# Kernel tuning notes

Hardware: AMD Instinct MI355X
Metric: run time of the kernel (lower is better)

The kernel has to match this reference:

```python
import jax, jax.numpy as jnp
import numpy as np

B, T, E, V, U = 4096, 80, 100, 10000, 1024


def setup_inputs() -> dict:
    key = jax.random.key(0)
    ks = jax.random.split(key, 8)
    def w(k, shape, fan_in):
        return jax.random.normal(k, shape, jnp.float32) * (1.0 / np.sqrt(fan_in))
    return {
        "inputs": jax.random.randint(ks[0], (B, T), 0, V, dtype=jnp.int32),
        "emb_table": w(ks[1], (V, E), E),
        "Wx0": w(ks[2], (E, U), E),
        "Wh0": w(ks[3], (U, U), U),
        "b0": jnp.zeros((U,), jnp.float32),
        "Wx1": w(ks[4], (U, U), U),
        "Wh1": w(ks[5], (U, U), U),
        "b1": jnp.zeros((U,), jnp.float32),
        "Wfc": w(ks[6], (U, 1), U),
        "bfc": jnp.zeros((1,), jnp.float32),
    }


def reference(inputs, emb_table, Wx0, Wh0, b0, Wx1, Wh1, b1, Wfc, bfc):
    # Embedding lookup: [B, T, E]
    x = emb_table[inputs]
    # Time-major for scan: [T, B, E]
    xs = jnp.swapaxes(x, 0, 1)
    h0_init = jnp.zeros((inputs.shape[0], Wh0.shape[0]), x.dtype)
    h1_init = jnp.zeros((inputs.shape[0], Wh1.shape[0]), x.dtype)

    def step(carry, xt):
        h0, h1 = carry
        # SimpleRNNCell: h' = tanh(x @ Wx + h @ Wh + b); output == new state
        h0 = jnp.tanh(xt @ Wx0 + h0 @ Wh0 + b0)
        h1 = jnp.tanh(h0 @ Wx1 + h1 @ Wh1 + b1)
        return (h0, h1), None

    (h0, h1), _ = jax.lax.scan(step, (h0_init, h1_init), xs)
    # Final dense + sigmoid on last layer-1 output
    prob = jax.nn.sigmoid(h1 @ Wfc + bfc)
    return prob
```

## Files before the change

kernel.cpp:

```cpp
#include <hip/hip_runtime.h>
#include <stdint.h>

#define B_ 4096
#define T_ 80
#define E_ 100
#define V_ 10000
#define U_ 1024

typedef unsigned short u16;
typedef __attribute__((ext_vector_type(8))) __bf16 bf16x8;
typedef __attribute__((ext_vector_type(4))) float f32x4;

__device__ __forceinline__ float bf2f(u16 u) {
    union { unsigned int i; float f; } v; v.i = ((unsigned int)u) << 16; return v.f;
}
__device__ __forceinline__ u16 f2bf(float f) {
    union { float f; unsigned int i; } v; v.f = f;
    unsigned int x = v.i;
    return (u16)((x + 0x7fffu + ((x >> 16) & 1u)) >> 16);
}

__device__ __forceinline__ void load16(const void* g, void* l) {
    __builtin_amdgcn_global_load_lds(
        (__attribute__((address_space(1))) void*)(uintptr_t)g,
        (__attribute__((address_space(3))) void*)(uint32_t)(uintptr_t)l,
        16, 0, 0);
}

__global__ void transpose_pad(const float* __restrict__ src, u16* __restrict__ dst,
                              int K, int N, int Kp)
{
    __shared__ u16 tile[32][33];
    const int k0 = blockIdx.x * 32;
    const int n0 = blockIdx.y * 32;
    const int tx = threadIdx.x & 31;
    const int ty = threadIdx.x >> 5;
#pragma unroll
    for (int i = 0; i < 4; i++) {
        int k = k0 + ty + i * 8;
        tile[ty + i * 8][tx] = (k < K) ? f2bf(src[(size_t)k * N + (n0 + tx)]) : (u16)0;
    }
    __syncthreads();
#pragma unroll
    for (int i = 0; i < 4; i++) {
        int n = n0 + ty + i * 8;
        dst[(size_t)n * Kp + (k0 + tx)] = tile[tx][ty + i * 8];
    }
}

__global__ void embed_pad(const float* __restrict__ emb, u16* __restrict__ dst)
{
    int id = blockIdx.x * 256 + threadIdx.x;
    int v = id >> 7, k = id & 127;
    dst[id] = (k < E_) ? f2bf(emb[v * E_ + k]) : (u16)0;
}

__global__ void __launch_bounds__(256, 2)
rnn_phase(const u16* __restrict__ embP, const int* __restrict__ idx,
          const u16* __restrict__ Wx0T, const u16* __restrict__ Wh0T, const float* __restrict__ b0,
          const u16* __restrict__ Wx1T, const u16* __restrict__ Wh1T, const float* __restrict__ b1,
          const u16* __restrict__ h0r, u16* __restrict__ h0w,
          const u16* __restrict__ h1r, u16* __restrict__ h1w,
          int do0, int do1)
{
    const int linear = blockIdx.x;
    const int layer  = linear >> 8;
    if (layer ? !do1 : !do0) return;

    __shared__ u16 As[2][128 * 64];
    __shared__ u16 Bs[2][128 * 64];
    const int tid  = threadIdx.x;
    const int lane = tid & 63;
    const int wave = tid >> 6;
    const int wm = wave >> 1, wn = wave & 1;
    const int sub = linear & 255;
    const int m0 = (sub & 31) * 128;
    const int n0 = (sub >> 5) * 128;

    const u16 *A1, *W1, *A2, *W2; const float* bias; u16* C; int K1; bool gather;
    if (layer == 0) { A1 = embP; W1 = Wx0T; K1 = 128;  gather = true;  A2 = h0r; W2 = Wh0T; bias = b0; C = h0w; }
    else            { A1 = h0r;  W1 = Wx1T; K1 = 1024; gather = false; A2 = h1r; W2 = Wh1T; bias = b1; C = h1w; }
    const int KB1 = K1 >> 6;
    const int TOT = KB1 + (U_ >> 6);

    const int r8 = lane >> 3;
    const int c8 = lane & 7;

    int gv[4];
    if (gather) {
#pragma unroll
        for (int cc = 0; cc < 4; cc++)
            gv[cc] = idx[(size_t)(m0 + wave * 32 + cc * 8 + r8) * T_];
    }

    const f32x4 z = {0.f, 0.f, 0.f, 0.f};
    f32x4 acc[4][4];
#pragma unroll
    for (int i = 0; i < 4; i++)
#pragma unroll
        for (int j = 0; j < 4; j++) acc[i][j] = z;

    const int l15 = lane & 15, q = lane >> 4, l7 = lane & 7;
    int offA[2][4], offB[2][4];
#pragma unroll
    for (int kk = 0; kk < 2; kk++) {
#pragma unroll
        for (int f = 0; f < 4; f++) {
            const int rA = wm * 64 + f * 16 + l15;
            const int rB = wn * 64 + f * 16 + l15;
            offA[kk][f] = rA * 64 + (((kk * 4 + q) ^ l7) * 8);
            offB[kk][f] = rB * 64 + (((kk * 4 + q) ^ l7) * 8);
        }
    }

    auto stage = [&](int u, int p) {
        u16* Ad = As[p] + wave * 2048;
        u16* Bd = Bs[p] + wave * 2048;
        if (u < KB1) {
            const int k0 = u * 64;
#pragma unroll
            for (int cc = 0; cc < 4; cc++) {
                const int row = wave * 32 + cc * 8 + r8;
                const int scw = (c8 ^ (row & 7)) * 8;
                const u16* ap = gather ? A1 + (size_t)gv[cc] * 128 + k0 + scw
                                       : A1 + (size_t)(m0 + row) * K1 + k0 + scw;
                load16(ap, Ad + cc * 512);
                load16(W1 + (size_t)(n0 + row) * K1 + k0 + scw, Bd + cc * 512);
            }
        } else {
            const int k0 = (u - KB1) * 64;
#pragma unroll
            for (int cc = 0; cc < 4; cc++) {
                const int row = wave * 32 + cc * 8 + r8;
                const int scw = (c8 ^ (row & 7)) * 8;
                load16(A2 + (size_t)(m0 + row) * U_ + k0 + scw, Ad + cc * 512);
                load16(W2 + (size_t)(n0 + row) * U_ + k0 + scw, Bd + cc * 512);
            }
        }
    };

    stage(0, 0);

#pragma unroll 1
    for (int u = 0; u < TOT; ++u) {
        const int p = u & 1;
        __syncthreads();
        if (u + 1 < TOT) stage(u + 1, p ^ 1);
#pragma unroll
        for (int kk = 0; kk < 2; kk++) {
            bf16x8 a[4], b[4];
#pragma unroll
            for (int f = 0; f < 4; f++) {
                a[f] = *reinterpret_cast<const bf16x8*>(As[p] + offA[kk][f]);
                b[f] = *reinterpret_cast<const bf16x8*>(Bs[p] + offB[kk][f]);
            }
#pragma unroll
            for (int i = 0; i < 4; i++)
#pragma unroll
                for (int j = 0; j < 4; j++)
                    acc[i][j] = __builtin_amdgcn_mfma_f32_16x16x32_bf16(a[i], b[j], acc[i][j], 0, 0, 0);
        }
    }

#pragma unroll
    for (int j = 0; j < 4; j++) {
        const int col = n0 + wn * 64 + j * 16 + l15;
        const float bv = bias[col];
#pragma unroll
        for (int i = 0; i < 4; i++) {
#pragma unroll
            for (int r = 0; r < 4; r++) {
                const int row = m0 + wm * 64 + i * 16 + (q << 2) + r;
                float x = acc[i][j][r] + bv;
                x = fminf(15.f, fmaxf(-15.f, x));
                float e = __expf(2.f * x);
                C[(size_t)row * U_ + col] = f2bf((e - 1.f) / (e + 1.f));
            }
        }
    }
}

__global__ void final_dense(const u16* __restrict__ h1, const float* __restrict__ Wfc,
                            const float* __restrict__ bfc, float* __restrict__ out)
{
    const int lane = threadIdx.x & 63;
    const int wave = threadIdx.x >> 6;
    const int row = blockIdx.x * 4 + wave;
    const u16* hp = h1 + (size_t)row * U_ + lane * 16;
    const float* wp = Wfc + lane * 16;
    float s = 0.f;
#pragma unroll
    for (int i = 0; i < 16; i++) s += bf2f(hp[i]) * wp[i];
#pragma unroll
    for (int off = 32; off; off >>= 1) s += __shfl_down(s, off);
    if (lane == 0) {
        float x = s + bfc[0];
        out[row] = 1.f / (1.f + __expf(-x));
    }
}

extern "C" void kernel_launch(void* const* d_in, const int* in_sizes, int n_in,
                              void* d_out, int out_size, void* d_ws, size_t ws_size,
                              hipStream_t stream)
{
    const int*   inputs = (const int*)d_in[0];
    const float* emb    = (const float*)d_in[1];
    const float* Wx0    = (const float*)d_in[2];
    const float* Wh0    = (const float*)d_in[3];
    const float* b0     = (const float*)d_in[4];
    const float* Wx1    = (const float*)d_in[5];
    const float* Wh1    = (const float*)d_in[6];
    const float* b1     = (const float*)d_in[7];
    const float* Wfc    = (const float*)d_in[8];
    const float* bfc    = (const float*)d_in[9];

    char* ws = (char*)d_ws;
    const size_t MB = 1 << 20;
    u16* h0b[2] = { (u16*)(ws + 0 * MB), (u16*)(ws + 8 * MB) };
    u16* h1b[2] = { (u16*)(ws + 16 * MB), (u16*)(ws + 24 * MB) };
    u16* embP = (u16*)(ws + 32 * MB);
    u16* Wx0T = (u16*)(ws + 35 * MB);
    u16* Wh0T = (u16*)(ws + 36 * MB);
    u16* Wx1T = (u16*)(ws + 38 * MB);
    u16* Wh1T = (u16*)(ws + 40 * MB);

    hipMemsetAsync(h0b[1], 0, 8 * MB, stream);
    hipMemsetAsync(h1b[1], 0, 8 * MB, stream);

    embed_pad<<<V_ * 128 / 256, 256, 0, stream>>>(emb, embP);
    transpose_pad<<<dim3(128 / 32, U_ / 32), 256, 0, stream>>>(Wx0, Wx0T, E_, U_, 128);
    transpose_pad<<<dim3(U_ / 32, U_ / 32), 256, 0, stream>>>(Wh0, Wh0T, U_, U_, U_);
    transpose_pad<<<dim3(U_ / 32, U_ / 32), 256, 0, stream>>>(Wx1, Wx1T, U_, U_, U_);
    transpose_pad<<<dim3(U_ / 32, U_ / 32), 256, 0, stream>>>(Wh1, Wh1T, U_, U_, U_);

    for (int p = 0; p <= T_; ++p) {
        const int e = p & 1;
        rnn_phase<<<512, 256, 0, stream>>>(embP, inputs + p,
                                           Wx0T, Wh0T, b0, Wx1T, Wh1T, b1,
                                           h0b[e ^ 1], h0b[e], h1b[e], h1b[e ^ 1],
                                           (int)(p < T_), (int)(p >= 1));
    }
    final_dense<<<B_ / 4, 256, 0, stream>>>(h1b[1], Wfc, bfc, (float*)d_out);
}
```

Before: 2.762 ms.

## Deepen GEMM pipeline to four LDS stages with K-tile 32 and explicit waitcnt

The K tile shrinks from 64 to 32 and the LDS ring grows from 2 to 4 buffers, keeping three tiles in flight ahead of compute. Each iteration waits only on the oldest outstanding async global-to-LDS loads via explicit vmcnt before a raw barrier, so memory latency overlaps with MFMA work. The XOR swizzle is redone for 32-wide rows. The cost is twice as many barriers per tile and fragile hand-counted vmcnt values that depend on the compiler's exact load count.

Result: slower. 3.320 ms (+20.2%).

```diff
diff --git a/kernel.cpp b/kernel.cpp
--- a/kernel.cpp
+++ b/kernel.cpp
@@ -67,8 +67,8 @@
     const int layer  = linear >> 8;
     if (layer ? !do1 : !do0) return;
 
-    __shared__ u16 As[2][128 * 64];
-    __shared__ u16 Bs[2][128 * 64];
+    __shared__ u16 As[4][128 * 32];
+    __shared__ u16 Bs[4][128 * 32];
     const int tid  = threadIdx.x;
     const int lane = tid & 63;
     const int wave = tid >> 6;
@@ -80,17 +80,17 @@
     const u16 *A1, *W1, *A2, *W2; const float* bias; u16* C; int K1; bool gather;
     if (layer == 0) { A1 = embP; W1 = Wx0T; K1 = 128;  gather = true;  A2 = h0r; W2 = Wh0T; bias = b0; C = h0w; }
     else            { A1 = h0r;  W1 = Wx1T; K1 = 1024; gather = false; A2 = h1r; W2 = Wh1T; bias = b1; C = h1w; }
-    const int KB1 = K1 >> 6;
-    const int TOT = KB1 + (U_ >> 6);
-
-    const int r8 = lane >> 3;
-    const int c8 = lane & 7;
-
-    int gv[4];
+    const int KB1 = K1 >> 5;
+    const int TOT = KB1 + (U_ >> 5);
+
+    const int r4 = lane >> 2;
+    const int c4 = lane & 3;
+
+    int gv[2];
     if (gather) {
 #pragma unroll
-        for (int cc = 0; cc < 4; cc++)
-            gv[cc] = idx[(size_t)(m0 + wave * 32 + cc * 8 + r8) * T_];
+        for (int cc = 0; cc < 2; cc++)
+            gv[cc] = idx[(size_t)(m0 + wave * 32 + cc * 16 + r4) * T_];
     }
 
     const f32x4 z = {0.f, 0.f, 0.f, 0.f};
@@ -100,66 +100,66 @@
 #pragma unroll
         for (int j = 0; j < 4; j++) acc[i][j] = z;
 
-    const int l15 = lane & 15, q = lane >> 4, l7 = lane & 7;
-    int offA[2][4], offB[2][4];
-#pragma unroll
-    for (int kk = 0; kk < 2; kk++) {
-#pragma unroll
-        for (int f = 0; f < 4; f++) {
-            const int rA = wm * 64 + f * 16 + l15;
-            const int rB = wn * 64 + f * 16 + l15;
-            offA[kk][f] = rA * 64 + (((kk * 4 + q) ^ l7) * 8);
-            offB[kk][f] = rB * 64 + (((kk * 4 + q) ^ l7) * 8);
-        }
-    }
-
-    auto stage = [&](int u, int p) {
-        u16* Ad = As[p] + wave * 2048;
-        u16* Bd = Bs[p] + wave * 2048;
+    const int l15 = lane & 15, q = lane >> 4;
+    int offA[4], offB[4];
+#pragma unroll
+    for (int f = 0; f < 4; f++) {
+        const int rA = wm * 64 + f * 16 + l15;
+        const int rB = wn * 64 + f * 16 + l15;
+        offA[f] = rA * 32 + ((q ^ ((rA + (rA >> 2)) & 3)) * 8);
+        offB[f] = rB * 32 + ((q ^ ((rB + (rB >> 2)) & 3)) * 8);
+    }
+
+    auto stage = [&](int u) {
+        const int slot = u & 3;
+        u16* Ad = As[slot] + wave * 1024;
+        u16* Bd = Bs[slot] + wave * 1024;
         if (u < KB1) {
-            const int k0 = u * 64;
-#pragma unroll
-            for (int cc = 0; cc < 4; cc++) {
-                const int row = wave * 32 + cc * 8 + r8;
-                const int scw = (c8 ^ (row & 7)) * 8;
-                const u16* ap = gather ? A1 + (size_t)gv[cc] * 128 + k0 + scw
-                                       : A1 + (size_t)(m0 + row) * K1 + k0 + scw;
+            const int k0 = u * 32;
+#pragma unroll
+            for (int cc = 0; cc < 2; cc++) {
+                const int row = wave * 32 + cc * 16 + r4;
+                const int sw  = ((c4 ^ ((row + (row >> 2)) & 3)) * 8);
+                const u16* ap = gather ? A1 + (size_t)gv[cc] * 128 + k0 + sw
+                                       : A1 + (size_t)(m0 + row) * K1 + k0 + sw;
                 load16(ap, Ad + cc * 512);
-                load16(W1 + (size_t)(n0 + row) * K1 + k0 + scw, Bd + cc * 512);
+                load16(W1 + (size_t)(n0 + row) * K1 + k0 + sw, Bd + cc * 512);
             }
         } else {
-            const int k0 = (u - KB1) * 64;
-#pragma unroll
-            for (int cc = 0; cc < 4; cc++) {
-                const int row = wave * 32 + cc * 8 + r8;
-                const int scw = (c8 ^ (row & 7)) * 8;
-                load16(A2 + (size_t)(m0 + row) * U_ + k0 + scw, Ad + cc * 512);
-                load16(W2 + (size_t)(n0 + row) * U_ + k0 + scw, Bd + cc * 512);
+            const int k0 = (u - KB1) * 32;
+#pragma unroll
+            for (int cc = 0; cc < 2; cc++) {
+                const int row = wave * 32 + cc * 16 + r4;
+                const int sw  = ((c4 ^ ((row + (row >> 2)) & 3)) * 8);
+                load16(A2 + (size_t)(m0 + row) * U_ + k0 + sw, Ad + cc * 512);
+                load16(W2 + (size_t)(n0 + row) * U_ + k0 + sw, Bd + cc * 512);
             }
         }
     };
 
-    stage(0, 0);
+    stage(0); stage(1); stage(2);
 
 #pragma unroll 1
     for (int u = 0; u < TOT; ++u) {
-        const int p = u & 1;
-        __syncthreads();
-        if (u + 1 < TOT) stage(u + 1, p ^ 1);
-#pragma unroll
-        for (int kk = 0; kk < 2; kk++) {
-            bf16x8 a[4], b[4];
-#pragma unroll
-            for (int f = 0; f < 4; f++) {
-                a[f] = *reinterpret_cast<const bf16x8*>(As[p] + offA[kk][f]);
-                b[f] = *reinterpret_cast<const bf16x8*>(Bs[p] + offB[kk][f]);
-            }
-#pragma unroll
-            for (int i = 0; i < 4; i++)
-#pragma unroll
-                for (int j = 0; j < 4; j++)
-                    acc[i][j] = __builtin_amdgcn_mfma_f32_16x16x32_bf16(a[i], b[j], acc[i][j], 0, 0, 0);
+        const int slot = u & 3;
+        if (u + 2 < TOT)      asm volatile("s_waitcnt vmcnt(8) lgkmcnt(0)" ::: "memory");
+        else if (u + 1 < TOT) asm volatile("s_waitcnt vmcnt(4) lgkmcnt(0)" ::: "memory");
+        else                  asm volatile("s_waitcnt vmcnt(0) lgkmcnt(0)" ::: "memory");
+        __builtin_amdgcn_s_barrier();
+        __builtin_amdgcn_sched_barrier(0);
+        if (u + 3 < TOT) stage(u + 3);
+
+        bf16x8 a[4], b[4];
+#pragma unroll
+        for (int f = 0; f < 4; f++) {
+            a[f] = *reinterpret_cast<const bf16x8*>(As[slot] + offA[f]);
+            b[f] = *reinterpret_cast<const bf16x8*>(Bs[slot] + offB[f]);
         }
+#pragma unroll
+        for (int i = 0; i < 4; i++)
+#pragma unroll
+            for (int j = 0; j < 4; j++)
+                acc[i][j] = __builtin_amdgcn_mfma_f32_16x16x32_bf16(a[i], b[j], acc[i][j], 0, 0, 0);
     }
 
 #pragma unroll
```

## Use 256x128 tiles with 512 threads and triple-buffered LDS pipeline

Applied to the files above, without the earlier changes.

Each block now uses 8 waves and a 256x128 output tile, so the grid shrinks to 256 blocks with the two layers interleaved by block index. The LDS ring grows from double to triple buffering, with explicit vmcnt waits and raw barriers so stages run two iterations ahead. The intent is to reuse each weight tile across more rows and hide global-to-LDS latency better. The cost is 144KB of LDS per block, one block per CU, and hand-counted vmcnt values that must match the number of loads issued per stage.

Result: slower. 3.208 ms (+16.1%).

```diff
diff --git a/kernel.cpp b/kernel.cpp
--- a/kernel.cpp
+++ b/kernel.cpp
@@ -55,7 +55,7 @@
     dst[id] = (k < E_) ? f2bf(emb[v * E_ + k]) : (u16)0;
 }
 
-__global__ void __launch_bounds__(256, 2)
+__global__ void __launch_bounds__(512, 1)
 rnn_phase(const u16* __restrict__ embP, const int* __restrict__ idx,
           const u16* __restrict__ Wx0T, const u16* __restrict__ Wh0T, const float* __restrict__ b0,
           const u16* __restrict__ Wx1T, const u16* __restrict__ Wh1T, const float* __restrict__ b1,
@@ -64,18 +64,18 @@
           int do0, int do1)
 {
     const int linear = blockIdx.x;
-    const int layer  = linear >> 8;
+    const int layer  = linear & 1;
     if (layer ? !do1 : !do0) return;
 
-    __shared__ u16 As[2][128 * 64];
-    __shared__ u16 Bs[2][128 * 64];
+    __shared__ u16 As[3][256 * 64];
+    __shared__ u16 Bs[3][128 * 64];
     const int tid  = threadIdx.x;
     const int lane = tid & 63;
     const int wave = tid >> 6;
     const int wm = wave >> 1, wn = wave & 1;
-    const int sub = linear & 255;
-    const int m0 = (sub & 31) * 128;
-    const int n0 = (sub >> 5) * 128;
+    const int sub = linear >> 1;
+    const int m0 = (sub & 15) * 256;
+    const int n0 = (sub >> 4) * 128;
 
     const u16 *A1, *W1, *A2, *W2; const float* bias; u16* C; int K1; bool gather;
     if (layer == 0) { A1 = embP; W1 = Wx0T; K1 = 128;  gather = true;  A2 = h0r; W2 = Wh0T; bias = b0; C = h0w; }
@@ -113,9 +113,10 @@
         }
     }
 
-    auto stage = [&](int u, int p) {
-        u16* Ad = As[p] + wave * 2048;
-        u16* Bd = Bs[p] + wave * 2048;
+    auto stage = [&](int u) {
+        const int slot = u % 3;
+        u16* Ad = As[slot] + wave * 2048;
+        u16* Bd = Bs[slot] + wave * 1024;
         if (u < KB1) {
             const int k0 = u * 64;
 #pragma unroll
@@ -125,6 +126,11 @@
                 const u16* ap = gather ? A1 + (size_t)gv[cc] * 128 + k0 + scw
                                        : A1 + (size_t)(m0 + row) * K1 + k0 + scw;
                 load16(ap, Ad + cc * 512);
+            }
+#pragma unroll
+            for (int cc = 0; cc < 2; cc++) {
+                const int row = wave * 16 + cc * 8 + r8;
+                const int scw = (c8 ^ (row & 7)) * 8;
                 load16(W1 + (size_t)(n0 + row) * K1 + k0 + scw, Bd + cc * 512);
             }
         } else {
@@ -134,25 +140,34 @@
                 const int row = wave * 32 + cc * 8 + r8;
                 const int scw = (c8 ^ (row & 7)) * 8;
                 load16(A2 + (size_t)(m0 + row) * U_ + k0 + scw, Ad + cc * 512);
+            }
+#pragma unroll
+            for (int cc = 0; cc < 2; cc++) {
+                const int row = wave * 16 + cc * 8 + r8;
+                const int scw = (c8 ^ (row & 7)) * 8;
                 load16(W2 + (size_t)(n0 + row) * U_ + k0 + scw, Bd + cc * 512);
             }
         }
     };
 
-    stage(0, 0);
+    stage(0); stage(1);
 
 #pragma unroll 1
     for (int u = 0; u < TOT; ++u) {
-        const int p = u & 1;
-        __syncthreads();
-        if (u + 1 < TOT) stage(u + 1, p ^ 1);
+        const int slot = u % 3;
+        if (u + 1 < TOT) asm volatile("s_waitcnt vmcnt(6)" ::: "memory");
+        else             asm volatile("s_waitcnt vmcnt(0)" ::: "memory");
+        __builtin_amdgcn_s_barrier();
+        __builtin_amdgcn_sched_barrier(0);
+        if (u + 2 < TOT) stage(u + 2);
+
 #pragma unroll
         for (int kk = 0; kk < 2; kk++) {
             bf16x8 a[4], b[4];
 #pragma unroll
             for (int f = 0; f < 4; f++) {
-                a[f] = *reinterpret_cast<const bf16x8*>(As[p] + offA[kk][f]);
-                b[f] = *reinterpret_cast<const bf16x8*>(Bs[p] + offB[kk][f]);
+                a[f] = *reinterpret_cast<const bf16x8*>(As[slot] + offA[kk][f]);
+                b[f] = *reinterpret_cast<const bf16x8*>(Bs[slot] + offB[kk][f]);
             }
 #pragma unroll
             for (int i = 0; i < 4; i++)
@@ -235,7 +250,7 @@
 
     for (int p = 0; p <= T_; ++p) {
         const int e = p & 1;
-        rnn_phase<<<512, 256, 0, stream>>>(embP, inputs + p,
+        rnn_phase<<<256, 512, 0, stream>>>(embP, inputs + p,
                                            Wx0T, Wh0T, b0, Wx1T, Wh1T, b1,
                                            h0b[e ^ 1], h0b[e], h1b[e], h1b[e ^ 1],
                                            (int)(p < T_), (int)(p >= 1));
```

## Load A operand directly from global into registers, keep only B in LDS

Applied to the files above, without the earlier changes.

The A tile (activations/embedding rows) is no longer staged through shared memory. Each lane loads its MFMA A fragments straight from global memory into registers, with double-buffered register sets. Only the weight tile B still goes through LDS, and the main loop is unrolled by two with ping-pong buffers. The aim is to halve LDS traffic and footprint, which may allow more occupancy. The cost is more register pressure, global loads that are less coalesced (16-byte per-lane row reads), and reliance on TOT being even.

New measurement: 5.350 ms. 1.94x slower.

```diff
diff --git a/kernel.cpp b/kernel.cpp
--- a/kernel.cpp
+++ b/kernel.cpp
@@ -67,7 +67,6 @@
     const int layer  = linear >> 8;
     if (layer ? !do1 : !do0) return;
 
-    __shared__ u16 As[2][128 * 64];
     __shared__ u16 Bs[2][128 * 64];
     const int tid  = threadIdx.x;
     const int lane = tid & 63;
@@ -86,13 +85,6 @@
     const int r8 = lane >> 3;
     const int c8 = lane & 7;
 
-    int gv[4];
-    if (gather) {
-#pragma unroll
-        for (int cc = 0; cc < 4; cc++)
-            gv[cc] = idx[(size_t)(m0 + wave * 32 + cc * 8 + r8) * T_];
-    }
-
     const f32x4 z = {0.f, 0.f, 0.f, 0.f};
     f32x4 acc[4][4];
 #pragma unroll
@@ -101,65 +93,89 @@
         for (int j = 0; j < 4; j++) acc[i][j] = z;
 
     const int l15 = lane & 15, q = lane >> 4, l7 = lane & 7;
-    int offA[2][4], offB[2][4];
+
+    const int colofs = q * 8;
+    const u16* Abase1[4];
+    const u16* Abase2[4];
+#pragma unroll
+    for (int f = 0; f < 4; f++) {
+        const int rowg = m0 + wm * 64 + f * 16 + l15;
+        Abase1[f] = gather ? A1 + (size_t)idx[(size_t)rowg * T_] * 128 + colofs
+                           : A1 + (size_t)rowg * K1 + colofs;
+        Abase2[f] = A2 + (size_t)rowg * U_ + colofs;
+    }
+
+    int offB[2][4];
 #pragma unroll
     for (int kk = 0; kk < 2; kk++) {
 #pragma unroll
         for (int f = 0; f < 4; f++) {
-            const int rA = wm * 64 + f * 16 + l15;
             const int rB = wn * 64 + f * 16 + l15;
-            offA[kk][f] = rA * 64 + (((kk * 4 + q) ^ l7) * 8);
             offB[kk][f] = rB * 64 + (((kk * 4 + q) ^ l7) * 8);
         }
     }
 
-    auto stage = [&](int u, int p) {
-        u16* Ad = As[p] + wave * 2048;
+    auto stageB = [&](int u, int p) {
         u16* Bd = Bs[p] + wave * 2048;
+        const u16* W    = (u < KB1) ? W1 : W2;
+        const int  kstr = (u < KB1) ? K1 : U_;
+        const int  k0   = (u < KB1) ? u * 64 : (u - KB1) * 64;
+#pragma unroll
+        for (int cc = 0; cc < 4; cc++) {
+            const int row = wave * 32 + cc * 8 + r8;
+            const int scw = (c8 ^ (row & 7)) * 8;
+            load16(W + (size_t)(n0 + row) * kstr + k0 + scw, Bd + cc * 512);
+        }
+    };
+
+    auto loadA = [&](int u, bf16x8 (&a)[8]) {
         if (u < KB1) {
             const int k0 = u * 64;
 #pragma unroll
-            for (int cc = 0; cc < 4; cc++) {
-                const int row = wave * 32 + cc * 8 + r8;
-                const int scw = (c8 ^ (row & 7)) * 8;
-                const u16* ap = gather ? A1 + (size_t)gv[cc] * 128 + k0 + scw
-                                       : A1 + (size_t)(m0 + row) * K1 + k0 + scw;
-                load16(ap, Ad + cc * 512);
-                load16(W1 + (size_t)(n0 + row) * K1 + k0 + scw, Bd + cc * 512);
+            for (int f = 0; f < 4; f++) {
+                const u16* rp = Abase1[f] + k0;
+                a[f]     = *reinterpret_cast<const bf16x8*>(rp);
+                a[4 + f] = *reinterpret_cast<const bf16x8*>(rp + 32);
             }
         } else {
             const int k0 = (u - KB1) * 64;
 #pragma unroll
-            for (int cc = 0; cc < 4; cc++) {
-                const int row = wave * 32 + cc * 8 + r8;
-                const int scw = (c8 ^ (row & 7)) * 8;
-                load16(A2 + (size_t)(m0 + row) * U_ + k0 + scw, Ad + cc * 512);
-                load16(W2 + (size_t)(n0 + row) * U_ + k0 + scw, Bd + cc * 512);
+            for (int f = 0; f < 4; f++) {
+                const u16* rp = Abase2[f] + k0;
+                a[f]     = *reinterpret_cast<const bf16x8*>(rp);
+                a[4 + f] = *reinterpret_cast<const bf16x8*>(rp + 32);
             }
         }
     };
 
-    stage(0, 0);
+    auto compute = [&](int p, const bf16x8 (&a)[8]) {
+#pragma unroll
+        for (int kk = 0; kk < 2; kk++) {
+            bf16x8 b[4];
+#pragma unroll
+            for (int f = 0; f < 4; f++)
+                b[f] = *reinterpret_cast<const bf16x8*>(Bs[p] + offB[kk][f]);
+#pragma unroll
+            for (int i = 0; i < 4; i++)
+#pragma unroll
+                for (int j = 0; j < 4; j++)
+                    acc[i][j] = __builtin_amdgcn_mfma_f32_16x16x32_bf16(a[kk * 4 + i], b[j], acc[i][j], 0, 0, 0);
+        }
+    };
+
+    bf16x8 aA[8], aB[8];
+    loadA(0, aA);
+    stageB(0, 0);
 
 #pragma unroll 1
-    for (int u = 0; u < TOT; ++u) {
-        const int p = u & 1;
+    for (int u = 0; u < TOT; u += 2) {
         __syncthreads();
-        if (u + 1 < TOT) stage(u + 1, p ^ 1);
-#pragma unroll
-        for (int kk = 0; kk < 2; kk++) {
-            bf16x8 a[4], b[4];
-#pragma unroll
-            for (int f = 0; f < 4; f++) {
-                a[f] = *reinterpret_cast<const bf16x8*>(As[p] + offA[kk][f]);
-                b[f] = *reinterpret_cast<const bf16x8*>(Bs[p] + offB[kk][f]);
-            }
-#pragma unroll
-            for (int i = 0; i < 4; i++)
-#pragma unroll
-                for (int j = 0; j < 4; j++)
-                    acc[i][j] = __builtin_amdgcn_mfma_f32_16x16x32_bf16(a[i], b[j], acc[i][j], 0, 0, 0);
-        }
+        stageB(u + 1, 1);
+        loadA(u + 1, aB);
+        compute(0, aA);
+        __syncthreads();
+        if (u + 2 < TOT) { stageB(u + 2, 0); loadA(u + 2, aA); }
+        compute(1, aB);
     }
 
 #pragma unroll
```
